# Performance work log

Hardware: AMD Instinct MI355X
Metric: run time of the kernel (lower is better)

Reference implementation:

```python
import jax, jax.numpy as jnp
import numpy as np

BG_W = 1.0
DILATED_BG_W = 5.0
EDGE_W = 20.0
KSIZE = 3


def setup_inputs() -> dict:
    key = jax.random.key(0)
    k1, k2 = jax.random.split(key)
    B, C, H, W = 16, 1, 1024, 1024
    pred = jax.random.normal(k1, (B, C, H, W), dtype=jnp.float32)
    target = (jax.random.uniform(k2, (B, C, H, W)) < 0.05).astype(jnp.float32)
    return {"pred": pred, "target": target}


def _dilate(target):
    # cv2.dilate with KSIZExKSIZE rect kernel == max pool, stride 1, SAME padding
    return jax.lax.reduce_window(
        target, -jnp.inf, jax.lax.max,
        window_dimensions=(1, 1, KSIZE, KSIZE),
        window_strides=(1, 1, 1, 1),
        padding="SAME",
    )


def reference(pred, target):
    dilated = _dilate(target)
    # weight: edge pixels (target>0.5) -> EDGE_W, else dilated band -> DILATED_BG_W, else BG_W
    weight = jnp.where(target > 0.5, EDGE_W,
                       jnp.where(dilated > 0.5, DILATED_BG_W, BG_W))
    # binary_cross_entropy_with_logits, reduction='none', then mean
    x = pred
    losses = weight * (jnp.maximum(x, 0.0) - x * target + jnp.log1p(jnp.exp(-jnp.abs(x))))
    return jnp.mean(losses)
```

## Files before the change

kernel.cpp:

```cpp
#include <hip/hip_runtime.h>

#define HH 1024
#define WW 1024

__device__ __forceinline__ float4 fmax4(float4 a, float4 b) {
    return make_float4(fmaxf(a.x, b.x), fmaxf(a.y, b.y),
                       fmaxf(a.z, b.z), fmaxf(a.w, b.w));
}

__device__ __forceinline__ float loss_elem(float x, float t, float dil) {
    float w = (t > 0.5f) ? 20.0f : ((dil > 0.5f) ? 5.0f : 1.0f);
    float a  = fabsf(x);
    float sp = __logf(1.0f + __expf(-a));
    return w * (fmaxf(x, 0.0f) - x * t + sp);
}

__global__ __launch_bounds__(256) void dilatedweightBCE_main(
        const float* __restrict__ pred,
        const float* __restrict__ target,
        float* __restrict__ partial) {
    __shared__ float swave[4];

    const int tid = threadIdx.x;
    const int h   = blockIdx.x;
    const int b   = blockIdx.y;
    const size_t rowbase = ((size_t)b * HH + h) * WW;

    const bool has_up = (h > 0);
    const bool has_dn = (h < HH - 1);

    float4 t0 = ((const float4*)(target + rowbase))[tid];
    float4 vm = t0;
    if (has_up) vm = fmax4(vm, ((const float4*)(target + rowbase - WW))[tid]);
    if (has_dn) vm = fmax4(vm, ((const float4*)(target + rowbase + WW))[tid]);
    float4 x = ((const float4*)(pred + rowbase))[tid];

    float l = __shfl_up(vm.w, 1);
    float r = __shfl_down(vm.x, 1);

    const int lane = tid & 63;
    const int c    = tid * 4;
    if (lane == 0) {
        l = 0.0f;
        if (c > 0) {
            float v = target[rowbase + c - 1];
            if (has_up) v = fmaxf(v, target[rowbase - WW + c - 1]);
            if (has_dn) v = fmaxf(v, target[rowbase + WW + c - 1]);
            l = v;
        }
    }
    if (lane == 63) {
        r = 0.0f;
        if (c + 4 < WW) {
            float v = target[rowbase + c + 4];
            if (has_up) v = fmaxf(v, target[rowbase - WW + c + 4]);
            if (has_dn) v = fmaxf(v, target[rowbase + WW + c + 4]);
            r = v;
        }
    }

    float d0 = fmaxf(l,    fmaxf(vm.x, vm.y));
    float d1 = fmaxf(vm.x, fmaxf(vm.y, vm.z));
    float d2 = fmaxf(vm.y, fmaxf(vm.z, vm.w));
    float d3 = fmaxf(vm.z, fmaxf(vm.w, r));

    float s = 0.0f;
    s += loss_elem(x.x, t0.x, d0);
    s += loss_elem(x.y, t0.y, d1);
    s += loss_elem(x.z, t0.z, d2);
    s += loss_elem(x.w, t0.w, d3);

    #pragma unroll
    for (int off = 32; off > 0; off >>= 1)
        s += __shfl_down(s, off);

    const int wave = tid >> 6;
    if (lane == 0) swave[wave] = s;
    __syncthreads();
    if (tid == 0) {
        partial[blockIdx.y * gridDim.x + blockIdx.x] =
            swave[0] + swave[1] + swave[2] + swave[3];
    }
}

__global__ __launch_bounds__(256) void dilatedweightBCE_reduce(
        const float* __restrict__ partial,
        float* __restrict__ out,
        int npart4,
        float inv_n) {
    __shared__ float swave[4];
    const int tid = threadIdx.x;

    float s = 0.0f;
    const float4* p4 = (const float4*)partial;
    for (int i = tid; i < npart4; i += 256) {
        float4 v = p4[i];
        s += v.x + v.y + v.z + v.w;
    }

    #pragma unroll
    for (int off = 32; off > 0; off >>= 1)
        s += __shfl_down(s, off);

    const int wave = tid >> 6;
    const int lane = tid & 63;
    if (lane == 0) swave[wave] = s;
    __syncthreads();
    if (tid == 0)
        out[0] = (swave[0] + swave[1] + swave[2] + swave[3]) * inv_n;
}

extern "C" void kernel_launch(void* const* d_in, const int* in_sizes, int n_in,
                              void* d_out, int out_size, void* d_ws, size_t ws_size,
                              hipStream_t stream) {
    const float* pred   = (const float*)d_in[0];
    const float* target = (const float*)d_in[1];
    float* out     = (float*)d_out;
    float* partial = (float*)d_ws;

    const int n  = in_sizes[0];
    const int Bn = n / (HH * WW);
    const int nblocks = HH * Bn;

    dim3 grid(HH, Bn);
    dilatedweightBCE_main<<<grid, 256, 0, stream>>>(pred, target, partial);
    dilatedweightBCE_reduce<<<1, 256, 0, stream>>>(partial, out,
                                                   nblocks / 4, 1.0f / (float)n);
}
```

Before: 162.1 us.

## Process eight rows per block with rolling target row registers

Each block now walks eight consecutive image rows and keeps the previous, current and next target rows in registers. Each target row is therefore loaded from memory about once instead of three times, and the grid and partial-sum count shrink by a factor of eight. In exchange there are fewer blocks, so less parallelism to hide latency, and the unrolled loop raises register use.

```diff
diff --git a/kernel.cpp b/kernel.cpp
--- a/kernel.cpp
+++ b/kernel.cpp
@@ -2,6 +2,8 @@
 
 #define HH 1024
 #define WW 1024
+#define W4 (WW / 4)
+#define ROWS 8
 
 __device__ __forceinline__ float4 fmax4(float4 a, float4 b) {
     return make_float4(fmaxf(a.x, b.x), fmaxf(a.y, b.y),
@@ -21,54 +23,68 @@
         float* __restrict__ partial) {
     __shared__ float swave[4];
 
-    const int tid = threadIdx.x;
-    const int h   = blockIdx.x;
-    const int b   = blockIdx.y;
-    const size_t rowbase = ((size_t)b * HH + h) * WW;
-
-    const bool has_up = (h > 0);
-    const bool has_dn = (h < HH - 1);
-
-    float4 t0 = ((const float4*)(target + rowbase))[tid];
-    float4 vm = t0;
-    if (has_up) vm = fmax4(vm, ((const float4*)(target + rowbase - WW))[tid]);
-    if (has_dn) vm = fmax4(vm, ((const float4*)(target + rowbase + WW))[tid]);
-    float4 x = ((const float4*)(pred + rowbase))[tid];
-
-    float l = __shfl_up(vm.w, 1);
-    float r = __shfl_down(vm.x, 1);
-
+    const int tid  = threadIdx.x;
     const int lane = tid & 63;
     const int c    = tid * 4;
-    if (lane == 0) {
-        l = 0.0f;
-        if (c > 0) {
-            float v = target[rowbase + c - 1];
-            if (has_up) v = fmaxf(v, target[rowbase - WW + c - 1]);
-            if (has_dn) v = fmaxf(v, target[rowbase + WW + c - 1]);
-            l = v;
-        }
-    }
-    if (lane == 63) {
-        r = 0.0f;
-        if (c + 4 < WW) {
-            float v = target[rowbase + c + 4];
-            if (has_up) v = fmaxf(v, target[rowbase - WW + c + 4]);
-            if (has_dn) v = fmaxf(v, target[rowbase + WW + c + 4]);
-            r = v;
-        }
-    }
+    const int b    = blockIdx.y;
+    const int h0   = blockIdx.x * ROWS;
 
-    float d0 = fmaxf(l,    fmaxf(vm.x, vm.y));
-    float d1 = fmaxf(vm.x, fmaxf(vm.y, vm.z));
-    float d2 = fmaxf(vm.y, fmaxf(vm.z, vm.w));
-    float d3 = fmaxf(vm.z, fmaxf(vm.w, r));
+    const float* timg = target + (size_t)b * HH * WW;
+    const float4* tg  = (const float4*)timg;
+    const float4* pg  = (const float4*)(pred + (size_t)b * HH * WW);
+
+    const float4 zero = make_float4(0.0f, 0.0f, 0.0f, 0.0f);
+    float4 t_prev = (h0 > 0) ? tg[(size_t)(h0 - 1) * W4 + tid] : zero;
+    float4 t_cur  = tg[(size_t)h0 * W4 + tid];
 
     float s = 0.0f;
-    s += loss_elem(x.x, t0.x, d0);
-    s += loss_elem(x.y, t0.y, d1);
-    s += loss_elem(x.z, t0.z, d2);
-    s += loss_elem(x.w, t0.w, d3);
+    #pragma unroll
+    for (int r = 0; r < ROWS; ++r) {
+        const int h = h0 + r;
+        const bool has_up = (h > 0);
+        const bool has_dn = (h < HH - 1);
+        const size_t rowoff = (size_t)h * WW;
+
+        float4 t_next = has_dn ? tg[(size_t)(h + 1) * W4 + tid] : zero;
+        float4 x      = pg[(size_t)h * W4 + tid];
+
+        float4 vm = fmax4(fmax4(t_prev, t_cur), t_next);
+
+        float l  = __shfl_up(vm.w, 1);
+        float rr = __shfl_down(vm.x, 1);
+
+        if (lane == 0) {
+            l = 0.0f;
+            if (c > 0) {
+                float v = timg[rowoff + c - 1];
+                if (has_up) v = fmaxf(v, timg[rowoff - WW + c - 1]);
+                if (has_dn) v = fmaxf(v, timg[rowoff + WW + c - 1]);
+                l = v;
+            }
+        }
+        if (lane == 63) {
+            rr = 0.0f;
+            if (c + 4 < WW) {
+                float v = timg[rowoff + c + 4];
+                if (has_up) v = fmaxf(v, timg[rowoff - WW + c + 4]);
+                if (has_dn) v = fmaxf(v, timg[rowoff + WW + c + 4]);
+                rr = v;
+            }
+        }
+
+        float d0 = fmaxf(l,    fmaxf(vm.x, vm.y));
+        float d1 = fmaxf(vm.x, fmaxf(vm.y, vm.z));
+        float d2 = fmaxf(vm.y, fmaxf(vm.z, vm.w));
+        float d3 = fmaxf(vm.z, fmaxf(vm.w, rr));
+
+        s += loss_elem(x.x, t_cur.x, d0);
+        s += loss_elem(x.y, t_cur.y, d1);
+        s += loss_elem(x.z, t_cur.z, d2);
+        s += loss_elem(x.w, t_cur.w, d3);
+
+        t_prev = t_cur;
+        t_cur  = t_next;
+    }
 
     #pragma unroll
     for (int off = 32; off > 0; off >>= 1)
@@ -120,9 +136,9 @@
 
     const int n  = in_sizes[0];
     const int Bn = n / (HH * WW);
-    const int nblocks = HH * Bn;
+    const int nblocks = (HH / ROWS) * Bn;
 
-    dim3 grid(HH, Bn);
+    dim3 grid(HH / ROWS, Bn);
     dilatedweightBCE_main<<<grid, 256, 0, stream>>>(pred, target, partial);
     dilatedweightBCE_reduce<<<1, 256, 0, stream>>>(partial, out,
                                                    nblocks / 4, 1.0f / (float)n);
```

Measured after the change: 162.6 us. No clear change (+0.3%).
